# Performance work log

Hardware: AMD Instinct MI355X
Metric: run time of the kernel (lower is better)

## Reference

```python
import jax, jax.numpy as jnp
import numpy as np

B, S, H = 8, 1024, 768      # batch, seq_len, encoder hidden
T, D = 9, 64                # output_type_size, att_dim
NEG = -1e12                 # masked_fill value from original code


def rope_tables(seq_len, dim):
    # theta_i = 10000^(-2i/dim), repeat_interleave(2) -> [t0,t0,t1,t1,...]
    pos = jnp.arange(seq_len, dtype=jnp.float32)[:, None]           # [S,1]
    theta = jnp.power(10000.0, -2.0 * jnp.arange(dim // 2, dtype=jnp.float32) / dim)
    theta = jnp.repeat(theta, 2)                                     # [D]
    ang = pos * theta[None, :]                                       # [S,D]
    return jnp.cos(ang), jnp.sin(ang)


def setup_inputs() -> dict:
    key = jax.random.key(0)
    k1, k2 = jax.random.split(key)
    hidden = jax.random.normal(k1, (B, S, H), dtype=jnp.float32)
    attention_mask = jnp.ones((B, S), dtype=jnp.int32)
    # xavier_normal-ish init for dense weight [2*T*D, H], zero bias
    fan = H + T * D * 2
    W = jax.random.normal(k2, (T * D * 2, H), dtype=jnp.float32) * (2.0 / fan) ** 0.5
    b = jnp.zeros((T * D * 2,), dtype=jnp.float32)
    return {"hidden": hidden, "attention_mask": attention_mask, "W": W, "b": b}


def reference(hidden, attention_mask, W, b):
    Bsz, Sl, _ = hidden.shape
    out = hidden @ W.T + b                          # [B,S,2*T*D]
    out = out.reshape(Bsz, Sl, T, D, 2)
    q = out[..., 0].transpose(0, 2, 1, 3)           # [B,T,S,D]
    k = out[..., 1].transpose(0, 2, 1, 3)           # [B,T,S,D]

    cos, sin = rope_tables(Sl, D)                   # [S,D] each

    def rot(x):
        # faithful to original: cat([-x[...,1::2], x[...,::2]], -1), NOT interleaved
        x2 = jnp.concatenate([-x[..., 1::2], x[..., ::2]], axis=-1)
        return x * cos + x2 * sin

    q, k = rot(q), rot(k)

    logits = jnp.einsum('btmd,btnd->btmn', q, k)    # [B,T,S,S]

    am = attention_mask.astype(bool)
    pad = am[:, None, :, None] & am[:, None, None, :]   # [B,1,S,S]
    triu = jnp.triu(jnp.ones((Sl, Sl), dtype=bool))     # spans i<=j
    return jnp.where(pad & triu, logits, NEG)
```

## Files before the change

kernel.cpp:

```cpp
#include <hip/hip_runtime.h>

#define S_LEN 1024
#define HID   768
#define T_SZ  9
#define NEG_VAL (-1e12f)

typedef __bf16 bf16x8 __attribute__((ext_vector_type(8)));
typedef float  f32x4  __attribute__((ext_vector_type(4)));
typedef short  short8 __attribute__((ext_vector_type(8)));
typedef short  short4v __attribute__((ext_vector_type(4)));
typedef float  float4v __attribute__((ext_vector_type(4)));

__device__ __forceinline__ unsigned short f2bf(float f) {
    unsigned int u = __builtin_bit_cast(unsigned int, f);
    u += 0x7FFFu + ((u >> 16) & 1u);
    return (unsigned short)(u >> 16);
}

__device__ __forceinline__ void gload_lds16(const void* g, void* l) {
    __builtin_amdgcn_global_load_lds(
        (const __attribute__((address_space(1))) unsigned int*)g,
        (__attribute__((address_space(3))) unsigned int*)l,
        16, 0, 0);
}

__device__ __forceinline__ void do_convert(const float* __restrict__ src,
                                           unsigned short* __restrict__ dst, int i) {
    float4v a = *((const float4v*)src + (size_t)i * 2);
    float4v b = *((const float4v*)src + (size_t)i * 2 + 1);
    short8 o;
    o[0] = (short)f2bf(a[0]); o[1] = (short)f2bf(a[1]);
    o[2] = (short)f2bf(a[2]); o[3] = (short)f2bf(a[3]);
    o[4] = (short)f2bf(b[0]); o[5] = (short)f2bf(b[1]);
    o[6] = (short)f2bf(b[2]); o[7] = (short)f2bf(b[3]);
    *(short8*)(dst + (size_t)i * 8) = o;
}

__global__ __launch_bounds__(256) void k_prep(
    const float* __restrict__ hidden, const float* __restrict__ W,
    unsigned short* __restrict__ hidB, unsigned short* __restrict__ wB,
    float* __restrict__ cosT, float* __restrict__ sinT, int n8h, int n8w)
{
    int i = blockIdx.x * 256 + threadIdx.x;
    if (i < n8h) { do_convert(hidden, hidB, i); return; }
    i -= n8h;
    if (i < n8w) { do_convert(W, wB, i); return; }
    i -= n8w;
    if (i < S_LEN * 64) {
        int s = i >> 6;
        int d = i & 63;
        float theta = exp2f(-13.2877123795f * (float)(d >> 1) * (1.0f / 32.0f));
        float ang = (float)s * theta;
        float sv, cv;
        sincosf(ang, &sv, &cv);
        cosT[i] = cv;
        sinT[i] = sv;
    }
}

union __align__(16) SmP {
    unsigned short buf[2][2][128 * 64];
    unsigned short Tr[128 * 136];
};

__global__ __launch_bounds__(256) void k_proj_fill(
    const unsigned short* __restrict__ hidB,
    const unsigned short* __restrict__ wB,
    const float* __restrict__ bias,
    const float* __restrict__ cosT,
    const float* __restrict__ sinT,
    unsigned short* __restrict__ qout,
    unsigned short* __restrict__ kout,
    float* __restrict__ out, int nproj)
{
    __shared__ SmP sm;
    int tid = threadIdx.x;
    int blk = blockIdx.x;

    if (blk >= nproj) {
        int f = blk - nproj;
        int bt = f / 28, rr = f % 28;
        int ti = 1; while (rr >= ti) { rr -= ti; ++ti; }
        size_t obase = ((size_t)bt * S_LEN + (size_t)ti * 128) * S_LEN + rr * 128;
        float4v nv = {NEG_VAL, NEG_VAL, NEG_VAL, NEG_VAL};
        #pragma unroll
        for (int it = 0; it < 16; ++it) {
            int idx = it * 256 + tid;
            int r = idx >> 5;
            int c4 = idx & 31;
            __builtin_nontemporal_store(nv, (float4v*)&out[obase + (size_t)r * S_LEN + c4 * 4]);
        }
        return;
    }

    int mt = blk / T_SZ;
    int t  = blk % T_SZ;
    int m0 = mt * 128;
    int n0 = t * 128;

    int lane = tid & 63;
    int wave = tid >> 6;
    int lr = lane & 15;
    int lq = lane >> 4;
    int wrow = wave * 32;

    float bv[8];
    #pragma unroll
    for (int fn = 0; fn < 8; ++fn) bv[fn] = bias[n0 + fn * 16 + lr];

    const unsigned short* aSrc[4];
    const unsigned short* bSrc[4];
    #pragma unroll
    for (int it = 0; it < 4; ++it) {
        int gsi = (wave * 4 + it) * 64 + lane;
        int r = gsi >> 3;
        int sw = gsi & 7;
        int seg8 = (sw ^ (r & 7)) << 3;
        aSrc[it] = hidB + (size_t)(m0 + r) * HID + seg8;
        bSrc[it] = wB  + (size_t)(n0 + r) * HID + seg8;
    }

    f32x4 acc[2][8];
    #pragma unroll
    for (int i = 0; i < 2; ++i)
        #pragma unroll
        for (int j = 0; j < 8; ++j) acc[i][j] = (f32x4){0.f, 0.f, 0.f, 0.f};

    #pragma unroll
    for (int it = 0; it < 4; ++it) {
        gload_lds16(aSrc[it], &sm.buf[0][0][(wave * 4 + it) * 512]);
        gload_lds16(bSrc[it], &sm.buf[0][1][(wave * 4 + it) * 512]);
    }
    __syncthreads();

    for (int kk = 0; kk < HID / 64; ++kk) {
        int par = kk & 1;
        if (kk < HID / 64 - 1) {
            #pragma unroll
            for (int it = 0; it < 4; ++it) {
                gload_lds16(aSrc[it] + (kk + 1) * 64, &sm.buf[par ^ 1][0][(wave * 4 + it) * 512]);
                gload_lds16(bSrc[it] + (kk + 1) * 64, &sm.buf[par ^ 1][1][(wave * 4 + it) * 512]);
            }
        }
        #pragma unroll
        for (int kb = 0; kb < 2; ++kb) {
            bf16x8 af[2];
            #pragma unroll
            for (int fm = 0; fm < 2; ++fm) {
                int r = wrow + fm * 16 + lr;
                int seg = kb * 4 + lq;
                af[fm] = *(const bf16x8*)&sm.buf[par][0][r * 64 + ((seg ^ (r & 7)) * 8)];
            }
            #pragma unroll
            for (int fn = 0; fn < 8; ++fn) {
                int r = fn * 16 + lr;
                int seg = kb * 4 + lq;
                bf16x8 bfr = *(const bf16x8*)&sm.buf[par][1][r * 64 + ((seg ^ (r & 7)) * 8)];
                acc[0][fn] = __builtin_amdgcn_mfma_f32_16x16x32_bf16(af[0], bfr, acc[0][fn], 0, 0, 0);
                acc[1][fn] = __builtin_amdgcn_mfma_f32_16x16x32_bf16(af[1], bfr, acc[1][fn], 0, 0, 0);
            }
        }
        __syncthreads();
    }

    #pragma unroll
    for (int fm = 0; fm < 2; ++fm) {
        #pragma unroll
        for (int fn = 0; fn < 8; ++fn) {
            int col = fn * 16 + lr;
            int r0 = wrow + fm * 16 + lq * 4;
            short4v pk;
            #pragma unroll
            for (int j = 0; j < 4; ++j) pk[j] = (short)f2bf(acc[fm][fn][j] + bv[fn]);
            *(short4v*)&sm.Tr[col * 136 + r0] = pk;
        }
    }
    __syncthreads();

    int d = tid & 63;
    int grp = tid >> 6;
    int cq = 2 * d, ck = 2 * d + 1;
    int pq = (d < 32) ? (4 * d + 2) : (4 * (d - 32));
    int pk2 = pq + 1;
    float sgn = (d < 32) ? -1.0f : 1.0f;
    #pragma unroll
    for (int ch = 0; ch < 4; ++ch) {
        int r0 = grp * 32 + ch * 8;
        bf16x8 xq = *(const bf16x8*)&sm.Tr[cq * 136 + r0];
        bf16x8 xk = *(const bf16x8*)&sm.Tr[ck * 136 + r0];
        bf16x8 yq = *(const bf16x8*)&sm.Tr[pq * 136 + r0];
        bf16x8 yk = *(const bf16x8*)&sm.Tr[pk2 * 136 + r0];
        #pragma unroll
        for (int rr = 0; rr < 8; ++rr) {
            int gm = m0 + r0 + rr;
            int s  = gm & (S_LEN - 1);
            int bb = gm >> 10;
            float cv = cosT[s * 64 + d];
            float sv = sinT[s * 64 + d];
            float qv = (float)xq[rr] * cv + sgn * (float)yq[rr] * sv;
            float kv = (float)xk[rr] * cv + sgn * (float)yk[rr] * sv;
            size_t ob = (((size_t)bb * T_SZ + t) * S_LEN + s) * 64 + d;
            qout[ob] = f2bf(qv);
            kout[ob] = f2bf(kv);
        }
    }
}

__global__ __launch_bounds__(256) void k_logits(
    const unsigned short* __restrict__ q,
    const unsigned short* __restrict__ k,
    const int* __restrict__ mask,
    float* __restrict__ out)
{
    __shared__ __align__(16) unsigned short As[128 * 64];
    __shared__ __align__(16) unsigned short Bs[128 * 64];
    __shared__ int mi[128], mj[128];

    int tid = threadIdx.x;
    int c = blockIdx.x;
    int bt = c / 36, r = c % 36;
    int ti = 0; while (r >= 8 - ti) { r -= 8 - ti; ++ti; }
    int tj = ti + r;
    size_t obase = ((size_t)bt * S_LEN + (size_t)ti * 128) * S_LEN + tj * 128;

    int b = bt / T_SZ;
    if (tid < 128) mi[tid] = mask[b * S_LEN + ti * 128 + tid];
    else           mj[tid - 128] = mask[b * S_LEN + tj * 128 + (tid - 128)];

    const unsigned short* qsrc = q + ((size_t)bt * S_LEN + (size_t)ti * 128) * 64;
    const unsigned short* ksrc = k + ((size_t)bt * S_LEN + (size_t)tj * 128) * 64;

    int lane = tid & 63;
    int wave = tid >> 6;
    #pragma unroll
    for (int it = 0; it < 4; ++it) {
        int gsi = (wave * 4 + it) * 64 + lane;
        int rr = gsi >> 3;
        int sw = gsi & 7;
        int off = rr * 64 + ((sw ^ (rr & 7)) << 3);
        gload_lds16(qsrc + off, &As[(wave * 4 + it) * 512]);
        gload_lds16(ksrc + off, &Bs[(wave * 4 + it) * 512]);
    }
    __syncthreads();

    int lr = lane & 15;
    int lq = lane >> 4;
    int wrow = wave * 32;

    f32x4 acc[2][8];
    #pragma unroll
    for (int i = 0; i < 2; ++i)
        #pragma unroll
        for (int j = 0; j < 8; ++j) acc[i][j] = (f32x4){0.f, 0.f, 0.f, 0.f};

    #pragma unroll
    for (int kb = 0; kb < 2; ++kb) {
        bf16x8 qf[2];
        #pragma unroll
        for (int fi = 0; fi < 2; ++fi) {
            int rr = wrow + fi * 16 + lr;
            int seg = kb * 4 + lq;
            qf[fi] = *(const bf16x8*)&As[rr * 64 + ((seg ^ (rr & 7)) * 8)];
        }
        #pragma unroll
        for (int fn = 0; fn < 8; ++fn) {
            int rr = fn * 16 + lr;
            int seg = kb * 4 + lq;
            bf16x8 kf = *(const bf16x8*)&Bs[rr * 64 + ((seg ^ (rr & 7)) * 8)];
            acc[0][fn] = __builtin_amdgcn_mfma_f32_16x16x32_bf16(kf, qf[0], acc[0][fn], 0, 0, 0);
            acc[1][fn] = __builtin_amdgcn_mfma_f32_16x16x32_bf16(kf, qf[1], acc[1][fn], 0, 0, 0);
        }
    }

    #pragma unroll
    for (int fi = 0; fi < 2; ++fi) {
        int il = wrow + fi * 16 + lr;
        int gi = ti * 128 + il;
        bool mrow = mi[il] != 0;
        size_t rbase = obase + (size_t)il * S_LEN;
        #pragma unroll
        for (int fn = 0; fn < 8; ++fn) {
            int j0 = fn * 16 + lq * 4;
            int gj0 = tj * 128 + j0;
            float4v v;
            #pragma unroll
            for (int e = 0; e < 4; ++e) {
                bool ok = mrow && (mj[j0 + e] != 0) && (gi <= gj0 + e);
                v[e] = ok ? acc[fi][fn][e] : NEG_VAL;
            }
            __builtin_nontemporal_store(v, (float4v*)&out[rbase + j0]);
        }
    }
}

extern "C" void kernel_launch(void* const* d_in, const int* in_sizes, int n_in,
                              void* d_out, int out_size, void* d_ws, size_t ws_size,
                              hipStream_t stream) {
    const float* hidden = (const float*)d_in[0];
    const int*   mask   = (const int*)d_in[1];
    const float* W      = (const float*)d_in[2];
    const float* bias   = (const float*)d_in[3];
    float* out = (float*)d_out;
    int Bsz = in_sizes[0] / (S_LEN * HID);

    char* ws = (char*)d_ws;
    float* cosT = (float*)ws;
    float* sinT = (float*)(ws + (size_t)S_LEN * 64 * 4);
    unsigned short* hidB = (unsigned short*)(ws + 2ull * S_LEN * 64 * 4);
    size_t hidElems = (size_t)Bsz * S_LEN * HID;
    unsigned short* wB = hidB + hidElems;
    size_t wElems = (size_t)2 * T_SZ * 64 * HID;
    unsigned short* qb = wB + wElems;
    size_t qkElems = (size_t)Bsz * T_SZ * S_LEN * 64;
    unsigned short* kb = qb + qkElems;

    int n8h = (int)(hidElems / 8);
    int n8w = (int)(wElems / 8);
    int nPrep = (n8h + n8w + S_LEN * 64 + 255) / 256;
    int nproj = Bsz * 72;
    int nfill = Bsz * T_SZ * 28;
    int ncomp = Bsz * T_SZ * 36;

    k_prep<<<dim3(nPrep), dim3(256), 0, stream>>>(hidden, W, hidB, wB, cosT, sinT, n8h, n8w);
    k_proj_fill<<<dim3(nproj + nfill), dim3(256), 0, stream>>>(hidB, wB, bias, cosT, sinT,
                                                               qb, kb, out, nproj);
    k_logits<<<dim3(ncomp), dim3(256), 0, stream>>>(qb, kb, mask, out);
}
```

Baseline: 381.7 us.

## Fuse fp32-to-bf16 conversion and RoPE into projection, merge fill into logits

Removes the separate prep kernel: the projection GEMM now loads fp32 hidden and W straight into registers, packs them to bf16 and writes them into LDS itself. The cos/sin tables are replaced by an in-register angle-addition recurrence. The masked fill is moved from the projection launch into the logits kernel, which now uses 128x256 tiles with whole-tile fill blocks. This drops a kernel launch and the bf16 workspace round trip. In exchange the async global-to-LDS loads become register loads plus conversion inside the GEMM loop, and the recurrence can drift slightly in precision.

```diff
diff --git a/kernel.cpp b/kernel.cpp
--- a/kernel.cpp
+++ b/kernel.cpp
@@ -17,6 +17,15 @@
     return (unsigned short)(u >> 16);
 }
 
+__device__ __forceinline__ short8 pack8(float4v a, float4v b) {
+    short8 o;
+    o[0] = (short)f2bf(a[0]); o[1] = (short)f2bf(a[1]);
+    o[2] = (short)f2bf(a[2]); o[3] = (short)f2bf(a[3]);
+    o[4] = (short)f2bf(b[0]); o[5] = (short)f2bf(b[1]);
+    o[6] = (short)f2bf(b[2]); o[7] = (short)f2bf(b[3]);
+    return o;
+}
+
 __device__ __forceinline__ void gload_lds16(const void* g, void* l) {
     __builtin_amdgcn_global_load_lds(
         (const __attribute__((address_space(1))) unsigned int*)g,
@@ -24,75 +33,21 @@
         16, 0, 0);
 }
 
-__device__ __forceinline__ void do_convert(const float* __restrict__ src,
-                                           unsigned short* __restrict__ dst, int i) {
-    float4v a = *((const float4v*)src + (size_t)i * 2);
-    float4v b = *((const float4v*)src + (size_t)i * 2 + 1);
-    short8 o;
-    o[0] = (short)f2bf(a[0]); o[1] = (short)f2bf(a[1]);
-    o[2] = (short)f2bf(a[2]); o[3] = (short)f2bf(a[3]);
-    o[4] = (short)f2bf(b[0]); o[5] = (short)f2bf(b[1]);
-    o[6] = (short)f2bf(b[2]); o[7] = (short)f2bf(b[3]);
-    *(short8*)(dst + (size_t)i * 8) = o;
-}
-
-__global__ __launch_bounds__(256) void k_prep(
-    const float* __restrict__ hidden, const float* __restrict__ W,
-    unsigned short* __restrict__ hidB, unsigned short* __restrict__ wB,
-    float* __restrict__ cosT, float* __restrict__ sinT, int n8h, int n8w)
-{
-    int i = blockIdx.x * 256 + threadIdx.x;
-    if (i < n8h) { do_convert(hidden, hidB, i); return; }
-    i -= n8h;
-    if (i < n8w) { do_convert(W, wB, i); return; }
-    i -= n8w;
-    if (i < S_LEN * 64) {
-        int s = i >> 6;
-        int d = i & 63;
-        float theta = exp2f(-13.2877123795f * (float)(d >> 1) * (1.0f / 32.0f));
-        float ang = (float)s * theta;
-        float sv, cv;
-        sincosf(ang, &sv, &cv);
-        cosT[i] = cv;
-        sinT[i] = sv;
-    }
-}
-
 union __align__(16) SmP {
     unsigned short buf[2][2][128 * 64];
     unsigned short Tr[128 * 136];
 };
 
-__global__ __launch_bounds__(256) void k_proj_fill(
-    const unsigned short* __restrict__ hidB,
-    const unsigned short* __restrict__ wB,
+__global__ __launch_bounds__(256) void k_proj(
+    const float* __restrict__ hidden,
+    const float* __restrict__ W,
     const float* __restrict__ bias,
-    const float* __restrict__ cosT,
-    const float* __restrict__ sinT,
     unsigned short* __restrict__ qout,
-    unsigned short* __restrict__ kout,
-    float* __restrict__ out, int nproj)
+    unsigned short* __restrict__ kout)
 {
     __shared__ SmP sm;
     int tid = threadIdx.x;
     int blk = blockIdx.x;
-
-    if (blk >= nproj) {
-        int f = blk - nproj;
-        int bt = f / 28, rr = f % 28;
-        int ti = 1; while (rr >= ti) { rr -= ti; ++ti; }
-        size_t obase = ((size_t)bt * S_LEN + (size_t)ti * 128) * S_LEN + rr * 128;
-        float4v nv = {NEG_VAL, NEG_VAL, NEG_VAL, NEG_VAL};
-        #pragma unroll
-        for (int it = 0; it < 16; ++it) {
-            int idx = it * 256 + tid;
-            int r = idx >> 5;
-            int c4 = idx & 31;
-            __builtin_nontemporal_store(nv, (float4v*)&out[obase + (size_t)r * S_LEN + c4 * 4]);
-        }
-        return;
-    }
-
     int mt = blk / T_SZ;
     int t  = blk % T_SZ;
     int m0 = mt * 128;
@@ -108,16 +63,16 @@
     #pragma unroll
     for (int fn = 0; fn < 8; ++fn) bv[fn] = bias[n0 + fn * 16 + lr];
 
-    const unsigned short* aSrc[4];
-    const unsigned short* bSrc[4];
+    const float* aP[4];
+    const float* bP[4];
     #pragma unroll
     for (int it = 0; it < 4; ++it) {
         int gsi = (wave * 4 + it) * 64 + lane;
         int r = gsi >> 3;
         int sw = gsi & 7;
         int seg8 = (sw ^ (r & 7)) << 3;
-        aSrc[it] = hidB + (size_t)(m0 + r) * HID + seg8;
-        bSrc[it] = wB  + (size_t)(n0 + r) * HID + seg8;
+        aP[it] = hidden + (size_t)(m0 + r) * HID + seg8;
+        bP[it] = W      + (size_t)(n0 + r) * HID + seg8;
     }
 
     f32x4 acc[2][8];
@@ -126,22 +81,33 @@
         #pragma unroll
         for (int j = 0; j < 8; ++j) acc[i][j] = (f32x4){0.f, 0.f, 0.f, 0.f};
 
+    float4v ar[4][2], br[4][2];
     #pragma unroll
     for (int it = 0; it < 4; ++it) {
-        gload_lds16(aSrc[it], &sm.buf[0][0][(wave * 4 + it) * 512]);
-        gload_lds16(bSrc[it], &sm.buf[0][1][(wave * 4 + it) * 512]);
-    }
-    __syncthreads();
+        ar[it][0] = *(const float4v*)(aP[it]);
+        ar[it][1] = *(const float4v*)(aP[it] + 4);
+        br[it][0] = *(const float4v*)(bP[it]);
+        br[it][1] = *(const float4v*)(bP[it] + 4);
+    }
 
     for (int kk = 0; kk < HID / 64; ++kk) {
         int par = kk & 1;
+        #pragma unroll
+        for (int it = 0; it < 4; ++it) {
+            int slot = ((wave * 4 + it) * 64 + lane) * 8;
+            *(short8*)&sm.buf[par][0][slot] = pack8(ar[it][0], ar[it][1]);
+            *(short8*)&sm.buf[par][1][slot] = pack8(br[it][0], br[it][1]);
+        }
         if (kk < HID / 64 - 1) {
             #pragma unroll
             for (int it = 0; it < 4; ++it) {
-                gload_lds16(aSrc[it] + (kk + 1) * 64, &sm.buf[par ^ 1][0][(wave * 4 + it) * 512]);
-                gload_lds16(bSrc[it] + (kk + 1) * 64, &sm.buf[par ^ 1][1][(wave * 4 + it) * 512]);
+                ar[it][0] = *(const float4v*)(aP[it] + (kk + 1) * 64);
+                ar[it][1] = *(const float4v*)(aP[it] + (kk + 1) * 64 + 4);
+                br[it][0] = *(const float4v*)(bP[it] + (kk + 1) * 64);
+                br[it][1] = *(const float4v*)(bP[it] + (kk + 1) * 64 + 4);
             }
         }
+        __syncthreads();
         #pragma unroll
         for (int kb = 0; kb < 2; ++kb) {
             bf16x8 af[2];
@@ -160,8 +126,8 @@
                 acc[1][fn] = __builtin_amdgcn_mfma_f32_16x16x32_bf16(af[1], bfr, acc[1][fn], 0, 0, 0);
             }
         }
-        __syncthreads();
-    }
+    }
+    __syncthreads();
 
     #pragma unroll
     for (int fm = 0; fm < 2; ++fm) {
@@ -183,6 +149,15 @@
     int pq = (d < 32) ? (4 * d + 2) : (4 * (d - 32));
     int pk2 = pq + 1;
     float sgn = (d < 32) ? -1.0f : 1.0f;
+
+    float theta = exp2f(-13.2877123795f * (float)(d >> 1) * (1.0f / 32.0f));
+    int sBase = (m0 & (S_LEN - 1)) + grp * 32;
+    int bb = m0 >> 10;
+    float cv, sv, ct, st;
+    __builtin_sincosf((float)sBase * theta, &sv, &cv);
+    __builtin_sincosf(theta, &st, &ct);
+    size_t obase = (((size_t)bb * T_SZ + t) * S_LEN + sBase) * 64 + d;
+
     #pragma unroll
     for (int ch = 0; ch < 4; ++ch) {
         int r0 = grp * 32 + ch * 8;
@@ -192,16 +167,14 @@
         bf16x8 yk = *(const bf16x8*)&sm.Tr[pk2 * 136 + r0];
         #pragma unroll
         for (int rr = 0; rr < 8; ++rr) {
-            int gm = m0 + r0 + rr;
-            int s  = gm & (S_LEN - 1);
-            int bb = gm >> 10;
-            float cv = cosT[s * 64 + d];
-            float sv = sinT[s * 64 + d];
             float qv = (float)xq[rr] * cv + sgn * (float)yq[rr] * sv;
             float kv = (float)xk[rr] * cv + sgn * (float)yk[rr] * sv;
-            size_t ob = (((size_t)bb * T_SZ + t) * S_LEN + s) * 64 + d;
+            size_t ob = obase + (size_t)(ch * 8 + rr) * 64;
             qout[ob] = f2bf(qv);
             kout[ob] = f2bf(kv);
+            float c2 = cv * ct - sv * st;
+            sv = sv * ct + cv * st;
+            cv = c2;
         }
     }
 }
@@ -212,23 +185,36 @@
     const int* __restrict__ mask,
     float* __restrict__ out)
 {
+    int tid = threadIdx.x;
+    int blk = blockIdx.x;
+    int bt  = blk >> 5;
+    int rem = blk & 31;
+    int ti  = rem >> 2;
+    int tj2 = rem & 3;
+    size_t obase = ((size_t)bt * S_LEN + (size_t)ti * 128) * S_LEN + (size_t)tj2 * 256;
+
+    if (ti >= 2 * tj2 + 2) {
+        float4v nv = {NEG_VAL, NEG_VAL, NEG_VAL, NEG_VAL};
+        #pragma unroll
+        for (int it = 0; it < 32; ++it) {
+            int idx = it * 256 + tid;
+            int r = idx >> 6;
+            int c4 = idx & 63;
+            __builtin_nontemporal_store(nv, (float4v*)&out[obase + (size_t)r * S_LEN + c4 * 4]);
+        }
+        return;
+    }
+
     __shared__ __align__(16) unsigned short As[128 * 64];
-    __shared__ __align__(16) unsigned short Bs[128 * 64];
-    __shared__ int mi[128], mj[128];
-
-    int tid = threadIdx.x;
-    int c = blockIdx.x;
-    int bt = c / 36, r = c % 36;
-    int ti = 0; while (r >= 8 - ti) { r -= 8 - ti; ++ti; }
-    int tj = ti + r;
-    size_t obase = ((size_t)bt * S_LEN + (size_t)ti * 128) * S_LEN + tj * 128;
+    __shared__ __align__(16) unsigned short Bs[256 * 64];
+    __shared__ int mi[128], mj[256];
 
     int b = bt / T_SZ;
     if (tid < 128) mi[tid] = mask[b * S_LEN + ti * 128 + tid];
-    else           mj[tid - 128] = mask[b * S_LEN + tj * 128 + (tid - 128)];
+    mj[tid] = mask[b * S_LEN + tj2 * 256 + tid];
 
     const unsigned short* qsrc = q + ((size_t)bt * S_LEN + (size_t)ti * 128) * 64;
-    const unsigned short* ksrc = k + ((size_t)bt * S_LEN + (size_t)tj * 128) * 64;
+    const unsigned short* ksrc = k + ((size_t)bt * S_LEN + (size_t)tj2 * 256) * 64;
 
     int lane = tid & 63;
     int wave = tid >> 6;
@@ -237,9 +223,14 @@
         int gsi = (wave * 4 + it) * 64 + lane;
         int rr = gsi >> 3;
         int sw = gsi & 7;
-        int off = rr * 64 + ((sw ^ (rr & 7)) << 3);
-        gload_lds16(qsrc + off, &As[(wave * 4 + it) * 512]);
-        gload_lds16(ksrc + off, &Bs[(wave * 4 + it) * 512]);
+        gload_lds16(qsrc + rr * 64 + ((sw ^ (rr & 7)) << 3), &As[(wave * 4 + it) * 512]);
+    }
+    #pragma unroll
+    for (int it = 0; it < 8; ++it) {
+        int gsi = (wave * 8 + it) * 64 + lane;
+        int rr = gsi >> 3;
+        int sw = gsi & 7;
+        gload_lds16(ksrc + rr * 64 + ((sw ^ (rr & 7)) << 3), &Bs[(wave * 8 + it) * 512]);
     }
     __syncthreads();
 
@@ -247,11 +238,11 @@
     int lq = lane >> 4;
     int wrow = wave * 32;
 
-    f32x4 acc[2][8];
+    f32x4 acc[2][16];
     #pragma unroll
     for (int i = 0; i < 2; ++i)
         #pragma unroll
-        for (int j = 0; j < 8; ++j) acc[i][j] = (f32x4){0.f, 0.f, 0.f, 0.f};
+        for (int j = 0; j < 16; ++j) acc[i][j] = (f32x4){0.f, 0.f, 0.f, 0.f};
 
     #pragma unroll
     for (int kb = 0; kb < 2; ++kb) {
@@ -263,7 +254,7 @@
             qf[fi] = *(const bf16x8*)&As[rr * 64 + ((seg ^ (rr & 7)) * 8)];
         }
         #pragma unroll
-        for (int fn = 0; fn < 8; ++fn) {
+        for (int fn = 0; fn < 16; ++fn) {
             int rr = fn * 16 + lr;
             int seg = kb * 4 + lq;
             bf16x8 kf = *(const bf16x8*)&Bs[rr * 64 + ((seg ^ (rr & 7)) * 8)];
@@ -279,9 +270,9 @@
         bool mrow = mi[il] != 0;
         size_t rbase = obase + (size_t)il * S_LEN;
         #pragma unroll
-        for (int fn = 0; fn < 8; ++fn) {
+        for (int fn = 0; fn < 16; ++fn) {
             int j0 = fn * 16 + lq * 4;
-            int gj0 = tj * 128 + j0;
+            int gj0 = tj2 * 256 + j0;
             float4v v;
             #pragma unroll
             for (int e = 0; e < 4; ++e) {
@@ -303,26 +294,13 @@
     float* out = (float*)d_out;
     int Bsz = in_sizes[0] / (S_LEN * HID);
 
-    char* ws = (char*)d_ws;
-    float* cosT = (float*)ws;
-    float* sinT = (float*)(ws + (size_t)S_LEN * 64 * 4);
-    unsigned short* hidB = (unsigned short*)(ws + 2ull * S_LEN * 64 * 4);
-    size_t hidElems = (size_t)Bsz * S_LEN * HID;
-    unsigned short* wB = hidB + hidElems;
-    size_t wElems = (size_t)2 * T_SZ * 64 * HID;
-    unsigned short* qb = wB + wElems;
+    unsigned short* qb = (unsigned short*)d_ws;
     size_t qkElems = (size_t)Bsz * T_SZ * S_LEN * 64;
     unsigned short* kb = qb + qkElems;
 
-    int n8h = (int)(hidElems / 8);
-    int n8w = (int)(wElems / 8);
-    int nPrep = (n8h + n8w + S_LEN * 64 + 255) / 256;
-    int nproj = Bsz * 72;
-    int nfill = Bsz * T_SZ * 28;
-    int ncomp = Bsz * T_SZ * 36;
-
-    k_prep<<<dim3(nPrep), dim3(256), 0, stream>>>(hidden, W, hidB, wB, cosT, sinT, n8h, n8w);
-    k_proj_fill<<<dim3(nproj + nfill), dim3(256), 0, stream>>>(hidB, wB, bias, cosT, sinT,
-                                                               qb, kb, out, nproj);
-    k_logits<<<dim3(ncomp), dim3(256), 0, stream>>>(qb, kb, mask, out);
-}
+    int nproj = Bsz * 8 * T_SZ;
+    int ntile = Bsz * T_SZ * 32;
+
+    k_proj<<<dim3(nproj), dim3(256), 0, stream>>>(hidden, W, bias, qb, kb);
+    k_logits<<<dim3(ntile), dim3(256), 0, stream>>>(qb, kb, mask, out);
+}
```

Result: slower. 398.7 us (+4.5%).
